# Optimization experiments

Hardware: AMD Instinct MI355X
Metric: run time of the kernel (lower is better)

The kernel has to match this reference:

```python
import jax, jax.numpy as jnp
import numpy as np

DIM = 1024
HEADS = 16
DIM_HEADS = DIM // HEADS  # 64
DIM_HIDDEN = DIM_HEADS * HEADS


def setup_inputs() -> dict:
    key = jax.random.key(0)
    k1, k2, k3, k4, k5 = jax.random.split(key, 5)
    b, t = 2, 2048
    x = jax.random.normal(k1, (b, t, DIM), dtype=jnp.float32)
    # torch nn.Linear weights are [out_features, in_features]
    s = DIM ** -0.5
    W_q = jax.random.normal(k2, (DIM_HIDDEN, DIM), dtype=jnp.float32) * s
    W_kv = jax.random.normal(k3, (2 * DIM_HIDDEN, DIM), dtype=jnp.float32) * s
    W_out = jax.random.normal(k4, (DIM, DIM_HIDDEN), dtype=jnp.float32) * s
    b_out = jax.random.normal(k5, (DIM,), dtype=jnp.float32) * 0.01
    return {"x": x, "W_q": W_q, "W_kv": W_kv, "W_out": W_out, "b_out": b_out}


def reference(x, W_q, W_kv, W_out, b_out):
    b, t, d = x.shape
    h, e = HEADS, DIM_HEADS
    # projections (Linear: x @ W.T)
    q = jnp.einsum('btd,fd->btf', x, W_q)
    kv = jnp.einsum('btd,fd->btf', x, W_kv)
    k, v = jnp.split(kv, 2, axis=-1)
    # split heads -> (b, h, t, e)
    split = lambda z: z.reshape(b, t, h, e).transpose(0, 2, 1, 3)
    q, k, v = split(q), split(k), split(v)
    # scaled dot-product attention; original uses exp/sum/div softmax
    scores = jnp.einsum('bhqe,bhke->bhqk', q, k) * (e ** -0.5)
    attn = jax.nn.softmax(scores, axis=-1)
    out = jnp.einsum('bhqk,bhke->bhqe', attn, v)
    out = out.transpose(0, 2, 1, 3).reshape(b, t, h * e)
    return jnp.einsum('btf,df->btd', out, W_out) + b_out
```

## Files before the change

kernel.cpp:

```cpp
#include <hip/hip_runtime.h>
#include <hip/hip_bf16.h>

#define BB   2
#define TT   2048
#define DD   1024
#define HH   16
#define EE   64
#define BT   4096

typedef __attribute__((ext_vector_type(8))) short bf16x8;
typedef __attribute__((ext_vector_type(4))) float floatx4;
typedef __attribute__((ext_vector_type(16))) float floatx16;

__device__ __forceinline__ unsigned short f2bf(float f) {
  unsigned int x = __float_as_uint(f);
  x += 0x7fffu + ((x >> 16) & 1u);
  return (unsigned short)(x >> 16);
}
__device__ __forceinline__ unsigned int pack2u(float a, float b) {
  union { __hip_bfloat162 h; unsigned int u; } r;
  r.h = __float22bfloat162_rn(make_float2(a, b));
  return r.u;
}
__device__ __forceinline__ uint4 pack8(const float4& a, const float4& b) {
  union { uint4 u; __hip_bfloat162 h[4]; } r;
  r.h[0] = __float22bfloat162_rn(make_float2(a.x, a.y));
  r.h[1] = __float22bfloat162_rn(make_float2(a.z, a.w));
  r.h[2] = __float22bfloat162_rn(make_float2(b.x, b.y));
  r.h[3] = __float22bfloat162_rn(make_float2(b.z, b.w));
  return r.u;
}
__device__ __forceinline__ void ld16(unsigned short* lds, const unsigned short* g) {
  __builtin_amdgcn_global_load_lds(
      (const __attribute__((address_space(1))) unsigned int*)g,
      (__attribute__((address_space(3))) unsigned int*)lds, 16, 0, 0);
}

#define GX   524288
#define GWQ  131072
#define GWKV 262144
#define GWO  131072

__global__ __launch_bounds__(256) void convert_kernel(
    const float* __restrict__ X,  const float* __restrict__ Wq,
    const float* __restrict__ Wkv, const float* __restrict__ Wout,
    unsigned short* __restrict__ Xb, unsigned short* __restrict__ Wb,
    unsigned short* __restrict__ Wob) {
  int g = blockIdx.x * 256 + threadIdx.x;
  const float* src; unsigned short* dst; int gi;
  if (g < GX)                        { src = X;    dst = Xb;  gi = g; }
  else if ((g -= GX) < GWQ)          { src = Wq;   dst = Wb;  gi = g; }
  else if ((g -= GWQ) < GWKV)        { src = Wkv;  dst = Wb + (size_t)GWQ * 8; gi = g; }
  else                               { src = Wout; dst = Wob; gi = g - GWKV; }
  const float4* s4 = reinterpret_cast<const float4*>(src) + (size_t)gi * 2;
  float4 a = s4[0], b = s4[1];
  reinterpret_cast<uint4*>(dst)[gi] = pack8(a, b);
}

__global__ __launch_bounds__(256) void gemm_qkv_mfma(
    const unsigned short* __restrict__ Xb,
    const unsigned short* __restrict__ Wb,
    unsigned short* __restrict__ Qh,
    unsigned short* __restrict__ Kh,
    unsigned short* __restrict__ Vt) {
  __shared__ __align__(16) unsigned short smem[128 * 136];
  unsigned short* As = smem;
  unsigned short* Bs = smem + 128 * 64;
  const int tid  = threadIdx.x;
  const int lane = tid & 63, w = tid >> 6;
  const int wm = w >> 1, wn = w & 1;
  const int q = lane >> 4, c = lane & 15;
  const int bm0 = blockIdx.y * 128;
  const int bn0 = blockIdx.x * 128;
  const unsigned short* Ag = Xb + (size_t)bm0 * DD;
  const unsigned short* Bg = Wb + (size_t)bn0 * DD;

  floatx4 acc[4][4];
#pragma unroll
  for (int i = 0; i < 4; ++i)
#pragma unroll
    for (int j = 0; j < 4; ++j) acc[i][j] = (floatx4){0.f, 0.f, 0.f, 0.f};

  int prow[4], pch[4];
#pragma unroll
  for (int t = 0; t < 4; ++t) {
    int s = (w * 4 + t) * 64 + lane;
    prow[t] = s >> 3;
    pch[t]  = (s & 7) ^ (prow[t] & 7);
  }
  int aoff[4][2], boff[4][2];
#pragma unroll
  for (int i = 0; i < 4; ++i)
#pragma unroll
    for (int h = 0; h < 2; ++h) {
      aoff[i][h] = (wm * 64 + i * 16 + c) * 64 + (((q + h * 4) ^ (c & 7)) << 3);
      boff[i][h] = (wn * 64 + i * 16 + c) * 64 + (((q + h * 4) ^ (c & 7)) << 3);
    }

  for (int kk = 0; kk < DD; kk += 64) {
    __syncthreads();
#pragma unroll
    for (int t = 0; t < 4; ++t) {
      int i = w * 4 + t;
      ld16(&As[i * 512], &Ag[(size_t)prow[t] * DD + kk + pch[t] * 8]);
      ld16(&Bs[i * 512], &Bg[(size_t)prow[t] * DD + kk + pch[t] * 8]);
    }
    __syncthreads();
    bf16x8 af[4][2], bfr[4][2];
#pragma unroll
    for (int i = 0; i < 4; ++i)
#pragma unroll
      for (int h = 0; h < 2; ++h) {
        af[i][h]  = *reinterpret_cast<const bf16x8*>(&As[aoff[i][h]]);
        bfr[i][h] = *reinterpret_cast<const bf16x8*>(&Bs[boff[i][h]]);
      }
#pragma unroll
    for (int i = 0; i < 4; ++i)
#pragma unroll
      for (int j = 0; j < 4; ++j) {
        acc[i][j] = __builtin_amdgcn_mfma_f32_16x16x32_bf16(af[i][0], bfr[j][0], acc[i][j], 0, 0, 0);
        acc[i][j] = __builtin_amdgcn_mfma_f32_16x16x32_bf16(af[i][1], bfr[j][1], acc[i][j], 0, 0, 0);
      }
  }

  const int region = bn0 >> 10;
  if (region < 2) {
    const float scl = (region == 0) ? 0.18033688011112042f : 1.0f;
#pragma unroll
    for (int i = 0; i < 4; ++i) {
#pragma unroll
      for (int j = 0; j < 4; ++j) {
#pragma unroll
        for (int reg = 0; reg < 4; ++reg) {
          int m = bm0 + wm * 64 + i * 16 + q * 4 + reg;
          int n = bn0 + wn * 64 + j * 16 + c;
          int nb = n & 1023;
          int h = nb >> 6, e = nb & 63;
          int b = m >> 11, t = m & 2047;
          unsigned short v = f2bf(acc[i][j][reg] * scl);
          if (region == 0) Qh[((size_t)((b * HH + h) * TT + t)) * EE + e] = v;
          else             Kh[((size_t)((b * HH + h) * TT + t)) * EE + e] = v;
        }
      }
    }
  } else {
    __syncthreads();
    unsigned short* tb = smem;
#pragma unroll
    for (int i = 0; i < 4; ++i) {
#pragma unroll
      for (int j = 0; j < 4; ++j) {
        int nl = wn * 64 + j * 16 + c;
        int ml = wm * 64 + i * 16 + q * 4;
        ushort4 pk;
        pk.x = f2bf(acc[i][j][0]);
        pk.y = f2bf(acc[i][j][1]);
        pk.z = f2bf(acc[i][j][2]);
        pk.w = f2bf(acc[i][j][3]);
        *reinterpret_cast<ushort4*>(&tb[nl * 136 + ml]) = pk;
      }
    }
    __syncthreads();
    const int b  = bm0 >> 11;
    const int t0 = bm0 & 2047;
    const int nb0 = bn0 & 1023;
    const int lr = tid & 15;
#pragma unroll
    for (int it = 0; it < 8; ++it) {
      int nl = it * 16 + (tid >> 4);
      int nb = nb0 + nl;
      int h = nb >> 6, e = nb & 63;
      uint4 vv = *reinterpret_cast<const uint4*>(&tb[nl * 136 + lr * 8]);
      *reinterpret_cast<uint4*>(
          &Vt[((size_t)(b * HH + h) * EE + e) * TT + t0 + lr * 8]) = vv;
    }
  }
}

#define CHUNK 16

__global__ __launch_bounds__(256) void attn_kernel(
    const unsigned short* __restrict__ Qh,
    const unsigned short* __restrict__ Kh,
    const unsigned short* __restrict__ Vtg,
    unsigned short* __restrict__ Aw) {
  __shared__ __align__(16) unsigned short smem[32768];

  const int tid  = threadIdx.x;
  const int lane = tid & 63;
  const int w    = tid >> 6;
  const int wv   = w & 1;
  const int p2   = w >> 1;
  const int n31  = lane & 31;
  const int g    = lane >> 5;

  const int flat = blockIdx.y * 16 + blockIdx.x;
  const int idx  = flat >> 3;
  const int bh   = (flat & 7) * 4 + (idx >> 4);
  const int qt   = idx & 15;
  const size_t base = (size_t)bh * TT * EE;
  const unsigned short* Qp = Qh + base + (size_t)(qt * 128 + wv * 64) * EE;
  const unsigned short* Kp = Kh + base;
  const unsigned short* Vp = Vtg + base;

  unsigned short* Kbuf = smem + p2 * 16384;
  unsigned short* Vbuf = smem + p2 * 16384 + 8192;

  bf16x8 qf[2][4];
#pragma unroll
  for (int s = 0; s < 2; ++s)
#pragma unroll
    for (int kc = 0; kc < 4; ++kc)
      qf[s][kc] = *reinterpret_cast<const bf16x8*>(
          &Qp[(size_t)(s * 32 + n31) * EE + kc * 16 + g * 8]);

  int srow[4], sch[4];
#pragma unroll
  for (int t = 0; t < 4; ++t) {
    int s = (t * 2 + wv) * 64 + lane;
    srow[t] = s >> 3;
    sch[t]  = (s & 7) ^ (srow[t] & 7);
  }

  floatx16 o_acc[2][2];
  o_acc[0][0] = (floatx16)(0.0f); o_acc[0][1] = (floatx16)(0.0f);
  o_acc[1][0] = (floatx16)(0.0f); o_acc[1][1] = (floatx16)(0.0f);
  float l_sum[2] = {0.0f, 0.0f};

  const int kt0 = p2 * CHUNK;
#pragma unroll
  for (int t = 0; t < 4; ++t) {
    ld16(&Kbuf[(t * 2 + wv) * 512], &Kp[(size_t)(kt0 * 64 + srow[t]) * EE + sch[t] * 8]);
    ld16(&Vbuf[(t * 2 + wv) * 512], &Vp[(size_t)srow[t] * TT + kt0 * 64 + sch[t] * 8]);
  }

  for (int kt = 0; kt < CHUNK; ++kt) {
    const int p  = kt & 1;
    const int gt = kt0 + ((kt + 1) & (CHUNK - 1));
#pragma unroll
    for (int t = 0; t < 4; ++t) {
      ld16(&Kbuf[(p ^ 1) * 4096 + (t * 2 + wv) * 512],
           &Kp[(size_t)(gt * 64 + srow[t]) * EE + sch[t] * 8]);
      ld16(&Vbuf[(p ^ 1) * 4096 + (t * 2 + wv) * 512],
           &Vp[(size_t)srow[t] * TT + gt * 64 + sch[t] * 8]);
    }
    asm volatile("s_waitcnt vmcnt(8)" ::: "memory");
    asm volatile("s_barrier" ::: "memory");

    const unsigned short* Kb = Kbuf + p * 4096;
    const unsigned short* Vb = Vbuf + p * 4096;

    bf16x8 kf[2][4];
#pragma unroll
    for (int nt = 0; nt < 2; ++nt) {
      const int krow = nt * 32 + n31;
#pragma unroll
      for (int kc = 0; kc < 4; ++kc) {
        const int swch = (kc * 2 + g) ^ (krow & 7);
        kf[nt][kc] = *reinterpret_cast<const bf16x8*>(&Kb[krow * 64 + swch * 8]);
      }
    }

#pragma unroll
    for (int s = 0; s < 2; ++s) {
      floatx16 sacc[2];
      sacc[0] = (floatx16)(0.0f);
      sacc[1] = (floatx16)(0.0f);
#pragma unroll
      for (int nt = 0; nt < 2; ++nt)
#pragma unroll
        for (int kc = 0; kc < 4; ++kc)
          sacc[nt] = __builtin_amdgcn_mfma_f32_32x32x16_bf16(kf[nt][kc], qf[s][kc], sacc[nt], 0, 0, 0);

      unsigned int pp[2][8] __attribute__((aligned(16)));
#pragma unroll
      for (int nt = 0; nt < 2; ++nt)
#pragma unroll
        for (int r = 0; r < 8; ++r) {
          float e0 = __builtin_amdgcn_exp2f(sacc[nt][2 * r]);
          float e1 = __builtin_amdgcn_exp2f(sacc[nt][2 * r + 1]);
          l_sum[s] += e0 + e1;
          pp[nt][r] = pack2u(e0, e1);
        }

#pragma unroll
      for (int nt = 0; nt < 2; ++nt)
#pragma unroll
        for (int kcp = 0; kcp < 2; ++kcp) {
          union { unsigned int u[4]; bf16x8 v; } pf;
          pf.u[0] = pp[nt][4 * kcp + 0]; pf.u[1] = pp[nt][4 * kcp + 1];
          pf.u[2] = pp[nt][4 * kcp + 2]; pf.u[3] = pp[nt][4 * kcp + 3];
#pragma unroll
          for (int eh = 0; eh < 2; ++eh) {
            const int vrow = eh * 32 + n31;
            const int c0 = (nt * 4 + 2 * kcp)     ^ (vrow & 7);
            const int c1 = (nt * 4 + 2 * kcp + 1) ^ (vrow & 7);
            uint2 v0 = *reinterpret_cast<const uint2*>(&Vb[vrow * 64 + c0 * 8 + g * 4]);
            uint2 v1 = *reinterpret_cast<const uint2*>(&Vb[vrow * 64 + c1 * 8 + g * 4]);
            union { unsigned int u[4]; bf16x8 v; } vf;
            vf.u[0] = v0.x; vf.u[1] = v0.y; vf.u[2] = v1.x; vf.u[3] = v1.y;
            o_acc[s][eh] = __builtin_amdgcn_mfma_f32_32x32x16_bf16(pf.v, vf.v, o_acc[s][eh], 0, 0, 0);
          }
        }
    }
    asm volatile("s_barrier" ::: "memory");
  }

  l_sum[0] += __shfl_xor(l_sum[0], 32, 64);
  l_sum[1] += __shfl_xor(l_sum[1], 32, 64);

  __syncthreads();
  float* fb = (float*)smem;
  if (p2 == 1) {
#pragma unroll
    for (int s = 0; s < 2; ++s) {
#pragma unroll
      for (int eh = 0; eh < 2; ++eh)
#pragma unroll
        for (int reg = 0; reg < 16; ++reg) {
          int qrl = (reg & 3) + 8 * (reg >> 2) + 4 * g;
          fb[wv * 4224 + (s * 32 + qrl) * 66 + eh * 32 + n31] = o_acc[s][eh][reg];
        }
      if (g == 0) fb[8448 + wv * 64 + s * 32 + n31] = l_sum[s];
    }
  }
  __syncthreads();
  if (p2 == 0) {
    const int b = bh >> 4, h = bh & 15;
#pragma unroll
    for (int s = 0; s < 2; ++s) {
      float linv[16];
#pragma unroll
      for (int reg = 0; reg < 16; ++reg) {
        int qrl = (reg & 3) + 8 * (reg >> 2) + 4 * g;
        float lown = __shfl(l_sum[s], qrl, 64);
        float lpar = fb[8448 + wv * 64 + s * 32 + qrl];
        linv[reg] = 1.0f / (lown + lpar);
      }
#pragma unroll
      for (int eh = 0; eh < 2; ++eh)
#pragma unroll
        for (int reg = 0; reg < 16; ++reg) {
          int qrl = (reg & 3) + 8 * (reg >> 2) + 4 * g;
          float o = o_acc[s][eh][reg] + fb[wv * 4224 + (s * 32 + qrl) * 66 + eh * 32 + n31];
          int t = qt * 128 + wv * 64 + s * 32 + qrl;
          Aw[((size_t)(b * TT + t)) * DD + h * EE + eh * 32 + n31] = f2bf(o * linv[reg]);
        }
    }
  }
}

__global__ __launch_bounds__(256) void gemm_out_mfma(
    const unsigned short* __restrict__ A,
    const unsigned short* __restrict__ Wob,
    const float* __restrict__ bias,
    float* __restrict__ out) {
  __shared__ __align__(16) unsigned short As[128 * 64];
  __shared__ __align__(16) unsigned short Bs[64 * 64];
  const int tid  = threadIdx.x;
  const int lane = tid & 63, w = tid >> 6;
  const int wm = w >> 1, wn = w & 1;
  const int q = lane >> 4, c = lane & 15;
  const int bm0 = blockIdx.y * 128;
  const int bn0 = blockIdx.x * 64;
  const unsigned short* Ag = A + (size_t)bm0 * DD;
  const unsigned short* Bg = Wob + (size_t)bn0 * DD;

  floatx4 acc[4][2];
#pragma unroll
  for (int i = 0; i < 4; ++i)
#pragma unroll
    for (int j = 0; j < 2; ++j) acc[i][j] = (floatx4){0.f, 0.f, 0.f, 0.f};

  int parow[4], pach[4];
#pragma unroll
  for (int t = 0; t < 4; ++t) {
    int s = (w * 4 + t) * 64 + lane;
    parow[t] = s >> 3;
    pach[t]  = (s & 7) ^ (parow[t] & 7);
  }
  int pbrow[2], pbch[2];
#pragma unroll
  for (int t = 0; t < 2; ++t) {
    int s = (w * 2 + t) * 64 + lane;
    pbrow[t] = s >> 3;
    pbch[t]  = (s & 7) ^ (pbrow[t] & 7);
  }

  for (int kk = 0; kk < DD; kk += 64) {
    __syncthreads();
#pragma unroll
    for (int t = 0; t < 4; ++t)
      ld16(&As[(w * 4 + t) * 512], &Ag[(size_t)parow[t] * DD + kk + pach[t] * 8]);
#pragma unroll
    for (int t = 0; t < 2; ++t)
      ld16(&Bs[(w * 2 + t) * 512], &Bg[(size_t)pbrow[t] * DD + kk + pbch[t] * 8]);
    __syncthreads();
    bf16x8 af[4][2], bfr[2][2];
#pragma unroll
    for (int h = 0; h < 2; ++h) {
      int ksw = ((q + h * 4) ^ (c & 7)) << 3;
#pragma unroll
      for (int i = 0; i < 4; ++i)
        af[i][h] = *reinterpret_cast<const bf16x8*>(&As[(wm * 64 + i * 16 + c) * 64 + ksw]);
#pragma unroll
      for (int j = 0; j < 2; ++j)
        bfr[j][h] = *reinterpret_cast<const bf16x8*>(&Bs[(wn * 32 + j * 16 + c) * 64 + ksw]);
    }
#pragma unroll
    for (int i = 0; i < 4; ++i)
#pragma unroll
      for (int j = 0; j < 2; ++j) {
        acc[i][j] = __builtin_amdgcn_mfma_f32_16x16x32_bf16(af[i][0], bfr[j][0], acc[i][j], 0, 0, 0);
        acc[i][j] = __builtin_amdgcn_mfma_f32_16x16x32_bf16(af[i][1], bfr[j][1], acc[i][j], 0, 0, 0);
      }
  }

#pragma unroll
  for (int i = 0; i < 4; ++i) {
#pragma unroll
    for (int j = 0; j < 2; ++j) {
      int n = bn0 + wn * 32 + j * 16 + c;
      float bv = bias[n];
#pragma unroll
      for (int reg = 0; reg < 4; ++reg) {
        int m = bm0 + wm * 64 + i * 16 + q * 4 + reg;
        out[(size_t)m * DD + n] = acc[i][j][reg] + bv;
      }
    }
  }
}

extern "C" void kernel_launch(void* const* d_in, const int* in_sizes, int n_in,
                              void* d_out, int out_size, void* d_ws, size_t ws_size,
                              hipStream_t stream) {
  const float* X    = (const float*)d_in[0];
  const float* Wq   = (const float*)d_in[1];
  const float* Wkv  = (const float*)d_in[2];
  const float* Wout = (const float*)d_in[3];
  const float* bout = (const float*)d_in[4];
  float* out = (float*)d_out;

  unsigned short* Qh  = (unsigned short*)d_ws;
  unsigned short* Kh  = Qh + (size_t)BT * DD;
  unsigned short* Vt  = Kh + (size_t)BT * DD;
  unsigned short* Aw  = Vt + (size_t)BT * DD;
  unsigned short* Xb  = Aw;
  unsigned short* Wb  = Aw + (size_t)BT * DD;
  unsigned short* Wob = Wb + (size_t)3 * 1024 * DD;

  convert_kernel<<<dim3(4096), 256, 0, stream>>>(X, Wq, Wkv, Wout, Xb, Wb, Wob);
  gemm_qkv_mfma<<<dim3(24, 32), 256, 0, stream>>>(Xb, Wb, Qh, Kh, Vt);
  attn_kernel<<<dim3(16, 32), 256, 0, stream>>>(Qh, Kh, Vt, Aw);
  gemm_out_mfma<<<dim3(16, 32), 256, 0, stream>>>(Aw, Wob, bout, out);
}
```

Before: 202.5 us.

## Restructure attention to 2-wave blocks over full key range, drop split-K merge

The attention kernel moves from 256-thread blocks, where two wave pairs each covered half of the keys and merged partial results through shared memory, to 128-thread blocks of two waves that each own 32 query rows and loop over all 32 key tiles. This removes the end-of-kernel LDS reduction and its extra barriers, halves shared memory and accumulator registers per block, and doubles the grid to 1024 blocks. In exchange, each block now loads K/V tiles for only 64 queries, so global K/V traffic per query is doubled. It also adds s_setprio around the MFMA sections to favour matrix work when waves compete.

Measured after the change: 201.2 us. Within noise of the previous version (-0.6%).

```diff
diff --git a/kernel.cpp b/kernel.cpp
--- a/kernel.cpp
+++ b/kernel.cpp
@@ -177,71 +177,66 @@
   }
 }
 
-#define CHUNK 16
-
-__global__ __launch_bounds__(256) void attn_kernel(
+#define NKT 32
+
+__global__ __launch_bounds__(128) void attn_kernel(
     const unsigned short* __restrict__ Qh,
     const unsigned short* __restrict__ Kh,
     const unsigned short* __restrict__ Vtg,
     unsigned short* __restrict__ Aw) {
-  __shared__ __align__(16) unsigned short smem[32768];
+  __shared__ __align__(16) unsigned short smem[16384];
 
   const int tid  = threadIdx.x;
   const int lane = tid & 63;
   const int w    = tid >> 6;
-  const int wv   = w & 1;
-  const int p2   = w >> 1;
   const int n31  = lane & 31;
   const int g    = lane >> 5;
 
-  const int flat = blockIdx.y * 16 + blockIdx.x;
+  const int flat = blockIdx.y * 32 + blockIdx.x;
   const int idx  = flat >> 3;
-  const int bh   = (flat & 7) * 4 + (idx >> 4);
-  const int qt   = idx & 15;
+  const int bh   = (flat & 7) * 4 + (idx >> 5);
+  const int qt   = idx & 31;
   const size_t base = (size_t)bh * TT * EE;
-  const unsigned short* Qp = Qh + base + (size_t)(qt * 128 + wv * 64) * EE;
+  const unsigned short* Qp = Qh + base + (size_t)(qt * 64 + w * 32) * EE;
   const unsigned short* Kp = Kh + base;
   const unsigned short* Vp = Vtg + base;
 
-  unsigned short* Kbuf = smem + p2 * 16384;
-  unsigned short* Vbuf = smem + p2 * 16384 + 8192;
-
-  bf16x8 qf[2][4];
-#pragma unroll
-  for (int s = 0; s < 2; ++s)
-#pragma unroll
-    for (int kc = 0; kc < 4; ++kc)
-      qf[s][kc] = *reinterpret_cast<const bf16x8*>(
-          &Qp[(size_t)(s * 32 + n31) * EE + kc * 16 + g * 8]);
+  unsigned short* Kbuf = smem;
+  unsigned short* Vbuf = smem + 8192;
+
+  bf16x8 qf[4];
+#pragma unroll
+  for (int kc = 0; kc < 4; ++kc)
+    qf[kc] = *reinterpret_cast<const bf16x8*>(
+        &Qp[(size_t)n31 * EE + kc * 16 + g * 8]);
 
   int srow[4], sch[4];
 #pragma unroll
   for (int t = 0; t < 4; ++t) {
-    int s = (t * 2 + wv) * 64 + lane;
+    int s = (t * 2 + w) * 64 + lane;
     srow[t] = s >> 3;
     sch[t]  = (s & 7) ^ (srow[t] & 7);
   }
 
-  floatx16 o_acc[2][2];
-  o_acc[0][0] = (floatx16)(0.0f); o_acc[0][1] = (floatx16)(0.0f);
-  o_acc[1][0] = (floatx16)(0.0f); o_acc[1][1] = (floatx16)(0.0f);
-  float l_sum[2] = {0.0f, 0.0f};
-
-  const int kt0 = p2 * CHUNK;
+  floatx16 o_acc[2];
+  o_acc[0] = (floatx16)(0.0f);
+  o_acc[1] = (floatx16)(0.0f);
+  float l_sum = 0.0f;
+
 #pragma unroll
   for (int t = 0; t < 4; ++t) {
-    ld16(&Kbuf[(t * 2 + wv) * 512], &Kp[(size_t)(kt0 * 64 + srow[t]) * EE + sch[t] * 8]);
-    ld16(&Vbuf[(t * 2 + wv) * 512], &Vp[(size_t)srow[t] * TT + kt0 * 64 + sch[t] * 8]);
-  }
-
-  for (int kt = 0; kt < CHUNK; ++kt) {
+    ld16(&Kbuf[(t * 2 + w) * 512], &Kp[(size_t)srow[t] * EE + sch[t] * 8]);
+    ld16(&Vbuf[(t * 2 + w) * 512], &Vp[(size_t)srow[t] * TT + sch[t] * 8]);
+  }
+
+  for (int kt = 0; kt < NKT; ++kt) {
     const int p  = kt & 1;
-    const int gt = kt0 + ((kt + 1) & (CHUNK - 1));
+    const int gt = (kt + 1) & (NKT - 1);
 #pragma unroll
     for (int t = 0; t < 4; ++t) {
-      ld16(&Kbuf[(p ^ 1) * 4096 + (t * 2 + wv) * 512],
+      ld16(&Kbuf[(p ^ 1) * 4096 + (t * 2 + w) * 512],
            &Kp[(size_t)(gt * 64 + srow[t]) * EE + sch[t] * 8]);
-      ld16(&Vbuf[(p ^ 1) * 4096 + (t * 2 + wv) * 512],
+      ld16(&Vbuf[(p ^ 1) * 4096 + (t * 2 + w) * 512],
            &Vp[(size_t)srow[t] * TT + gt * 64 + sch[t] * 8]);
     }
     asm volatile("s_waitcnt vmcnt(8)" ::: "memory");
@@ -261,93 +256,72 @@
       }
     }
 
-#pragma unroll
-    for (int s = 0; s < 2; ++s) {
-      floatx16 sacc[2];
-      sacc[0] = (floatx16)(0.0f);
-      sacc[1] = (floatx16)(0.0f);
-#pragma unroll
-      for (int nt = 0; nt < 2; ++nt)
-#pragma unroll
-        for (int kc = 0; kc < 4; ++kc)
-          sacc[nt] = __builtin_amdgcn_mfma_f32_32x32x16_bf16(kf[nt][kc], qf[s][kc], sacc[nt], 0, 0, 0);
-
-      unsigned int pp[2][8] __attribute__((aligned(16)));
-#pragma unroll
-      for (int nt = 0; nt < 2; ++nt)
-#pragma unroll
-        for (int r = 0; r < 8; ++r) {
-          float e0 = __builtin_amdgcn_exp2f(sacc[nt][2 * r]);
-          float e1 = __builtin_amdgcn_exp2f(sacc[nt][2 * r + 1]);
-          l_sum[s] += e0 + e1;
-          pp[nt][r] = pack2u(e0, e1);
+    floatx16 sacc[2];
+    sacc[0] = (floatx16)(0.0f);
+    sacc[1] = (floatx16)(0.0f);
+    __builtin_amdgcn_s_setprio(1);
+#pragma unroll
+    for (int nt = 0; nt < 2; ++nt)
+#pragma unroll
+      for (int kc = 0; kc < 4; ++kc)
+        sacc[nt] = __builtin_amdgcn_mfma_f32_32x32x16_bf16(kf[nt][kc], qf[kc], sacc[nt], 0, 0, 0);
+    __builtin_amdgcn_s_setprio(0);
+
+    unsigned int pp[2][8] __attribute__((aligned(16)));
+#pragma unroll
+    for (int nt = 0; nt < 2; ++nt)
+#pragma unroll
+      for (int r = 0; r < 8; ++r) {
+        float e0 = __builtin_amdgcn_exp2f(sacc[nt][2 * r]);
+        float e1 = __builtin_amdgcn_exp2f(sacc[nt][2 * r + 1]);
+        l_sum += e0 + e1;
+        pp[nt][r] = pack2u(e0, e1);
+      }
+
+    __builtin_amdgcn_s_setprio(1);
+#pragma unroll
+    for (int nt = 0; nt < 2; ++nt)
+#pragma unroll
+      for (int kcp = 0; kcp < 2; ++kcp) {
+        union { unsigned int u[4]; bf16x8 v; } pf;
+        pf.u[0] = pp[nt][4 * kcp + 0]; pf.u[1] = pp[nt][4 * kcp + 1];
+        pf.u[2] = pp[nt][4 * kcp + 2]; pf.u[3] = pp[nt][4 * kcp + 3];
+#pragma unroll
+        for (int eh = 0; eh < 2; ++eh) {
+          const int vrow = eh * 32 + n31;
+          const int c0 = (nt * 4 + 2 * kcp)     ^ (vrow & 7);
+          const int c1 = (nt * 4 + 2 * kcp + 1) ^ (vrow & 7);
+          uint2 v0 = *reinterpret_cast<const uint2*>(&Vb[vrow * 64 + c0 * 8 + g * 4]);
+          uint2 v1 = *reinterpret_cast<const uint2*>(&Vb[vrow * 64 + c1 * 8 + g * 4]);
+          union { unsigned int u[4]; bf16x8 v; } vf;
+          vf.u[0] = v0.x; vf.u[1] = v0.y; vf.u[2] = v1.x; vf.u[3] = v1.y;
+          o_acc[eh] = __builtin_amdgcn_mfma_f32_32x32x16_bf16(pf.v, vf.v, o_acc[eh], 0, 0, 0);
         }
-
-#pragma unroll
-      for (int nt = 0; nt < 2; ++nt)
-#pragma unroll
-        for (int kcp = 0; kcp < 2; ++kcp) {
-          union { unsigned int u[4]; bf16x8 v; } pf;
-          pf.u[0] = pp[nt][4 * kcp + 0]; pf.u[1] = pp[nt][4 * kcp + 1];
-          pf.u[2] = pp[nt][4 * kcp + 2]; pf.u[3] = pp[nt][4 * kcp + 3];
-#pragma unroll
-          for (int eh = 0; eh < 2; ++eh) {
-            const int vrow = eh * 32 + n31;
-            const int c0 = (nt * 4 + 2 * kcp)     ^ (vrow & 7);
-            const int c1 = (nt * 4 + 2 * kcp + 1) ^ (vrow & 7);
-            uint2 v0 = *reinterpret_cast<const uint2*>(&Vb[vrow * 64 + c0 * 8 + g * 4]);
-            uint2 v1 = *reinterpret_cast<const uint2*>(&Vb[vrow * 64 + c1 * 8 + g * 4]);
-            union { unsigned int u[4]; bf16x8 v; } vf;
-            vf.u[0] = v0.x; vf.u[1] = v0.y; vf.u[2] = v1.x; vf.u[3] = v1.y;
-            o_acc[s][eh] = __builtin_amdgcn_mfma_f32_32x32x16_bf16(pf.v, vf.v, o_acc[s][eh], 0, 0, 0);
-          }
-        }
-    }
+      }
+    __builtin_amdgcn_s_setprio(0);
     asm volatile("s_barrier" ::: "memory");
   }
 
-  l_sum[0] += __shfl_xor(l_sum[0], 32, 64);
-  l_sum[1] += __shfl_xor(l_sum[1], 32, 64);
-
-  __syncthreads();
-  float* fb = (float*)smem;
-  if (p2 == 1) {
-#pragma unroll
-    for (int s = 0; s < 2; ++s) {
-#pragma unroll
-      for (int eh = 0; eh < 2; ++eh)
-#pragma unroll
-        for (int reg = 0; reg < 16; ++reg) {
-          int qrl = (reg & 3) + 8 * (reg >> 2) + 4 * g;
-          fb[wv * 4224 + (s * 32 + qrl) * 66 + eh * 32 + n31] = o_acc[s][eh][reg];
-        }
-      if (g == 0) fb[8448 + wv * 64 + s * 32 + n31] = l_sum[s];
-    }
-  }
-  __syncthreads();
-  if (p2 == 0) {
-    const int b = bh >> 4, h = bh & 15;
-#pragma unroll
-    for (int s = 0; s < 2; ++s) {
-      float linv[16];
-#pragma unroll
-      for (int reg = 0; reg < 16; ++reg) {
-        int qrl = (reg & 3) + 8 * (reg >> 2) + 4 * g;
-        float lown = __shfl(l_sum[s], qrl, 64);
-        float lpar = fb[8448 + wv * 64 + s * 32 + qrl];
-        linv[reg] = 1.0f / (lown + lpar);
-      }
-#pragma unroll
-      for (int eh = 0; eh < 2; ++eh)
-#pragma unroll
-        for (int reg = 0; reg < 16; ++reg) {
-          int qrl = (reg & 3) + 8 * (reg >> 2) + 4 * g;
-          float o = o_acc[s][eh][reg] + fb[wv * 4224 + (s * 32 + qrl) * 66 + eh * 32 + n31];
-          int t = qt * 128 + wv * 64 + s * 32 + qrl;
-          Aw[((size_t)(b * TT + t)) * DD + h * EE + eh * 32 + n31] = f2bf(o * linv[reg]);
-        }
-    }
-  }
+  asm volatile("s_waitcnt vmcnt(0)" ::: "memory");
+
+  l_sum += __shfl_xor(l_sum, 32, 64);
+
+  const int b = bh >> 4, h = bh & 15;
+  float linv[16];
+#pragma unroll
+  for (int reg = 0; reg < 16; ++reg) {
+    int qrl = (reg & 3) + 8 * (reg >> 2) + 4 * g;
+    linv[reg] = 1.0f / __shfl(l_sum, qrl, 64);
+  }
+#pragma unroll
+  for (int eh = 0; eh < 2; ++eh)
+#pragma unroll
+    for (int reg = 0; reg < 16; ++reg) {
+      int qrl = (reg & 3) + 8 * (reg >> 2) + 4 * g;
+      int t = qt * 64 + w * 32 + qrl;
+      Aw[((size_t)(b * TT + t)) * DD + h * EE + eh * 32 + n31] =
+          f2bf(o_acc[eh][reg] * linv[reg]);
+    }
 }
 
 __global__ __launch_bounds__(256) void gemm_out_mfma(
@@ -451,6 +425,6 @@
 
   convert_kernel<<<dim3(4096), 256, 0, stream>>>(X, Wq, Wkv, Wout, Xb, Wb, Wob);
   gemm_qkv_mfma<<<dim3(24, 32), 256, 0, stream>>>(Xb, Wb, Qh, Kh, Vt);
-  attn_kernel<<<dim3(16, 32), 256, 0, stream>>>(Qh, Kh, Vt, Aw);
+  attn_kernel<<<dim3(32, 32), 128, 0, stream>>>(Qh, Kh, Vt, Aw);
   gemm_out_mfma<<<dim3(16, 32), 256, 0, stream>>>(Aw, Wob, bout, out);
 }
```
